# Optimization experiments

Hardware: AMD Instinct MI355X
Metric: run time of the kernel (lower is better)

Reference implementation:

```python
import jax, jax.numpy as jnp
import numpy as np

B, S, D, H = 2, 2048, 1024, 16
DK = D // H  # 64

def setup_inputs() -> dict:
    key = jax.random.key(0)
    ks = jax.random.split(key, 8)
    xavier = np.sqrt(6.0 / (D + D))  # xavier_uniform bound for square Linear
    def lin_w(k):
        return jax.random.uniform(k, (D, D), jnp.float32, -xavier, xavier)
    return {
        'Q': jax.random.normal(ks[0], (B, S, D), jnp.float32),
        'length': jax.random.randint(ks[1], (B,), 1, S + 1, jnp.int32),
        'Wq': lin_w(ks[2]), 'bq': jnp.zeros((D,), jnp.float32),
        'Wk': lin_w(ks[3]), 'bk': jnp.zeros((D,), jnp.float32),
        'Wv': lin_w(ks[4]), 'bv': jnp.zeros((D,), jnp.float32),
    }

def reference(Q, length, Wq, bq, Wk, bk, Wv, bv):
    # project and split heads: [B,S,D] -> [B,H,S,DK]
    def heads(x, W, b):
        y = jnp.einsum('bsd,de->bse', x, W) + b
        return y.reshape(B, S, H, DK).transpose(0, 2, 1, 3)
    q = heads(Q, Wq, bq)
    k = heads(Q, Wk, bk)
    v = heads(Q, Wv, bv)
    scores = jnp.einsum('bhqd,bhkd->bhqk', q, k) / np.sqrt(DK)
    scores = jnp.exp(scores)  # NOTE: raw exp, no max-subtraction (faithful)
    # multiplicative key mask: mask[b,k] = k < length[b], broadcast over q,h
    mask = (jnp.arange(S)[None, :] < length[:, None]).astype(scores.dtype)
    scores = scores * mask[:, None, None, :]
    attn = scores / (jnp.sum(scores, axis=-1, keepdims=True) + 1e-8)
    ctx = jnp.einsum('bhqk,bhkd->bhqd', attn, v)
    return ctx.transpose(0, 2, 1, 3).reshape(B, S, D)
```

## Files before the change

kernel.cpp:

```cpp
#include <hip/hip_runtime.h>
#include <hip/hip_bf16.h>

#define B_  2
#define S_  2048
#define D_  1024
#define H_  16
#define DK_ 64
#define M_  (B_ * S_)

typedef short short8 __attribute__((ext_vector_type(8)));
typedef float float4v __attribute__((ext_vector_type(4)));

static __device__ __forceinline__ ushort f32_to_bf16bits(float f) {
    union { __hip_bfloat16 h; ushort u; } cv;
    cv.h = __float2bfloat16(f);
    return cv.u;
}

static __device__ __forceinline__ void glds16(const ushort* g, ushort* l) {
    __builtin_amdgcn_global_load_lds(
        (const __attribute__((address_space(1))) unsigned int*)g,
        (__attribute__((address_space(3))) unsigned int*)l, 16, 0, 0);
}

__global__ __launch_bounds__(256) void prep(
    const float* __restrict__ X, const float* __restrict__ W0,
    const float* __restrict__ W1, const float* __restrict__ W2,
    ushort* __restrict__ Xb, ushort* __restrict__ Wt)
{
    const int z = blockIdx.z;
    const int t = threadIdx.x;

    if (z >= 3) {
        const int blk = (z - 3) * 256 + blockIdx.y * 16 + blockIdx.x;
        const int i = blk * 2048 + t * 8;
        float4v a = *(const float4v*)(X + i);
        float4v b = *(const float4v*)(X + i + 4);
        short8 o;
        o[0] = (short)f32_to_bf16bits(a[0]); o[1] = (short)f32_to_bf16bits(a[1]);
        o[2] = (short)f32_to_bf16bits(a[2]); o[3] = (short)f32_to_bf16bits(a[3]);
        o[4] = (short)f32_to_bf16bits(b[0]); o[5] = (short)f32_to_bf16bits(b[1]);
        o[6] = (short)f32_to_bf16bits(b[2]); o[7] = (short)f32_to_bf16bits(b[3]);
        *(short8*)(Xb + i) = o;
        return;
    }

    const float* W = (z == 0) ? W0 : ((z == 1) ? W1 : W2);
    ushort* out = Wt + (size_t)z * D_ * D_;

    __shared__ ushort tile[64 * 72];
    int n0 = blockIdx.x * 64, k0 = blockIdx.y * 64;
    int r = t >> 3, g = t & 7;

    #pragma unroll
    for (int p = 0; p < 2; ++p) {
        int rr = r + p * 32;
        const float* src = W + (size_t)(k0 + rr) * D_ + n0 + g * 8;
        float4v a = *(const float4v*)src;
        float4v b = *(const float4v*)(src + 4);
        short8 o;
        o[0] = (short)f32_to_bf16bits(a[0]); o[1] = (short)f32_to_bf16bits(a[1]);
        o[2] = (short)f32_to_bf16bits(a[2]); o[3] = (short)f32_to_bf16bits(a[3]);
        o[4] = (short)f32_to_bf16bits(b[0]); o[5] = (short)f32_to_bf16bits(b[1]);
        o[6] = (short)f32_to_bf16bits(b[2]); o[7] = (short)f32_to_bf16bits(b[3]);
        *(short8*)&tile[rr * 72 + g * 8] = o;
    }
    __syncthreads();
    #pragma unroll
    for (int p = 0; p < 2; ++p) {
        int rr = r + p * 32;
        short8 v;
        #pragma unroll
        for (int i = 0; i < 8; ++i)
            v[i] = (short)tile[(g * 8 + i) * 72 + rr];
        *(short8*)(out + (size_t)(n0 + rr) * D_ + k0 + g * 8) = v;
    }
}

__global__ __launch_bounds__(256) void proj_gemm(
    const ushort* __restrict__ X,
    const ushort* __restrict__ Wt,
    const float* __restrict__ b0, const float* __restrict__ b1,
    const float* __restrict__ b2,
    const int* __restrict__ length,
    ushort* __restrict__ qkv)
{
    const int z = blockIdx.z;
    const int m0 = blockIdx.x * 64, n0 = blockIdx.y * 128;

    if (z >= 1) {
        const int bidx = m0 >> 11;
        const int s0 = m0 & (S_ - 1);
        if (s0 >= length[bidx]) return;
    }

    const ushort* Wtz  = Wt + (size_t)z * D_ * D_;
    const float* bias = (z == 0) ? b0 : ((z == 1) ? b1 : b2);
    ushort* out = qkv + (size_t)z * M_ * D_;

    __shared__ ushort As[64 * 64];
    __shared__ ushort Bs[128 * 64];

    const int t = threadIdx.x;
    const int lane = t & 63, wid = t >> 6;
    const int quad = lane >> 4, l16 = lane & 15;
    const int wr = wid >> 1, wc = wid & 1;

    float4v acc[2][4] = {};

    for (int k0 = 0; k0 < D_; k0 += 64) {
        __syncthreads();
        #pragma unroll
        for (int j = 0; j < 2; ++j) {
            const int cid = wid * 128 + j * 64 + lane;
            const int row = cid >> 3;
            const int cl  = (cid & 7) ^ (row & 7);
            glds16(X + (size_t)(m0 + row) * D_ + k0 + cl * 8, &As[cid * 8]);
        }
        #pragma unroll
        for (int j = 0; j < 4; ++j) {
            const int cid = wid * 256 + j * 64 + lane;
            const int row = cid >> 3;
            const int cl  = (cid & 7) ^ (row & 7);
            glds16(Wtz + (size_t)(n0 + row) * D_ + k0 + cl * 8, &Bs[cid * 8]);
        }
        __syncthreads();

        #pragma unroll
        for (int ks = 0; ks < 2; ++ks) {
            short8 a[2], bb[4];
            #pragma unroll
            for (int i = 0; i < 2; ++i) {
                const int r = wr * 32 + i * 16 + l16;
                const int ph = (ks * 4 + quad) ^ (r & 7);
                a[i] = *(short8*)&As[r * 64 + ph * 8];
            }
            #pragma unroll
            for (int j = 0; j < 4; ++j) {
                const int r = wc * 64 + j * 16 + l16;
                const int ph = (ks * 4 + quad) ^ (r & 7);
                bb[j] = *(short8*)&Bs[r * 64 + ph * 8];
            }
            #pragma unroll
            for (int i = 0; i < 2; ++i)
                #pragma unroll
                for (int j = 0; j < 4; ++j)
                    acc[i][j] = __builtin_amdgcn_mfma_f32_16x16x32_bf16(
                        a[i], bb[j], acc[i][j], 0, 0, 0);
        }
    }

    #pragma unroll
    for (int j = 0; j < 4; ++j) {
        const int col = n0 + wc * 64 + j * 16 + l16;
        const float bv = bias[col];
        const int h = col >> 6, dk = col & (DK_ - 1);
        #pragma unroll
        for (int i = 0; i < 2; ++i) {
            #pragma unroll
            for (int rr = 0; rr < 4; ++rr) {
                const int row = m0 + wr * 32 + i * 16 + quad * 4 + rr;
                const int bidx = row >> 11;
                const int s = row & (S_ - 1);
                const float v = acc[i][j][rr] + bv;
                size_t addr;
                if (z == 2)
                    addr = ((size_t)(bidx * H_ + h) * DK_ + dk) * S_ + s;
                else
                    addr = ((size_t)(bidx * H_ + h) * S_ + s) * DK_ + dk;
                out[addr] = f32_to_bf16bits(v);
            }
        }
    }
}

__global__ __launch_bounds__(256) void attention(
    const ushort* __restrict__ qkv, const int* __restrict__ length,
    float* __restrict__ out)
{
    const int b = blockIdx.z, h = blockIdx.y, q0 = blockIdx.x * 64;
    int len = length[b];
    if (len > S_) len = S_;
    if (len < 1) len = 1;
    const int nkt = (len + 63) >> 6;

    const ushort* qb = qkv + ((size_t)(b * H_ + h) * S_ + q0) * DK_;
    const ushort* kb = qkv + (size_t)M_ * D_ + (size_t)(b * H_ + h) * S_ * DK_;
    const ushort* vb = qkv + (size_t)2 * M_ * D_ + (size_t)(b * H_ + h) * DK_ * S_;

    __shared__ ushort Qs[64 * 64];
    __shared__ ushort Ks[64 * 64];
    __shared__ ushort Vs[64 * 64];
    __shared__ ushort Ps[64 * 64];

    const int t = threadIdx.x, lane = t & 63, wid = t >> 6;
    const int quad = lane >> 4, l16 = lane & 15;
    const int qr = wid * 16 + l16;

    #pragma unroll
    for (int j = 0; j < 2; ++j) {
        const int cid = wid * 128 + j * 64 + lane;
        const int row = cid >> 3;
        const int cl  = (cid & 7) ^ (row & 7);
        glds16(qb + (size_t)row * DK_ + cl * 8, &Qs[cid * 8]);
    }

    float4v cacc[4] = {};
    float rs[4] = {};

    for (int kt = 0; kt < nkt; ++kt) {
        __syncthreads();
        #pragma unroll
        for (int j = 0; j < 2; ++j) {
            const int cid = wid * 128 + j * 64 + lane;
            const int row = cid >> 3;
            const int cl  = (cid & 7) ^ (row & 7);
            glds16(kb + (size_t)(kt * 64 + row) * DK_ + cl * 8, &Ks[cid * 8]);
            glds16(vb + (size_t)row * S_ + kt * 64 + cl * 8,    &Vs[cid * 8]);
        }
        __syncthreads();

        float4v sacc[4] = {};
        #pragma unroll
        for (int ks = 0; ks < 2; ++ks) {
            const int pha = (ks * 4 + quad) ^ (qr & 7);
            short8 a = *(short8*)&Qs[qr * 64 + pha * 8];
            #pragma unroll
            for (int ct = 0; ct < 4; ++ct) {
                const int kr = ct * 16 + l16;
                const int phb = (ks * 4 + quad) ^ (kr & 7);
                short8 bb = *(short8*)&Ks[kr * 64 + phb * 8];
                sacc[ct] = __builtin_amdgcn_mfma_f32_16x16x32_bf16(
                    a, bb, sacc[ct], 0, 0, 0);
            }
        }

        #pragma unroll
        for (int ct = 0; ct < 4; ++ct) {
            const int key = kt * 64 + ct * 16 + l16;
            const int c   = ct * 2 + (l16 >> 3);
            #pragma unroll
            for (int rr = 0; rr < 4; ++rr) {
                const int prow = wid * 16 + quad * 4 + rr;
                float val = 0.f;
                if (key < len) val = __expf(sacc[ct][rr] * 0.125f);
                rs[rr] += val;
                const int ph = c ^ (prow & 7);
                Ps[prow * 64 + ph * 8 + (l16 & 7)] = f32_to_bf16bits(val);
            }
        }

        #pragma unroll
        for (int ks = 0; ks < 2; ++ks) {
            const int pha = (ks * 4 + quad) ^ (qr & 7);
            short8 ap = *(short8*)&Ps[qr * 64 + pha * 8];
            #pragma unroll
            for (int ct = 0; ct < 4; ++ct) {
                const int vr = ct * 16 + l16;
                const int phb = (ks * 4 + quad) ^ (vr & 7);
                short8 vv = *(short8*)&Vs[vr * 64 + phb * 8];
                cacc[ct] = __builtin_amdgcn_mfma_f32_16x16x32_bf16(
                    ap, vv, cacc[ct], 0, 0, 0);
            }
        }
    }

    #pragma unroll
    for (int rr = 0; rr < 4; ++rr) {
        float v = rs[rr];
        #pragma unroll
        for (int off = 1; off < 16; off <<= 1)
            v += __shfl_xor(v, off, 16);
        rs[rr] = v;
    }

    #pragma unroll
    for (int ct = 0; ct < 4; ++ct)
        #pragma unroll
        for (int rr = 0; rr < 4; ++rr) {
            const int q = q0 + wid * 16 + quad * 4 + rr;
            const int d = h * 64 + ct * 16 + l16;
            out[((size_t)b * S_ + q) * D_ + d] = cacc[ct][rr] / (rs[rr] + 1e-8f);
        }
}

extern "C" void kernel_launch(void* const* d_in, const int* in_sizes, int n_in,
                              void* d_out, int out_size, void* d_ws, size_t ws_size,
                              hipStream_t stream)
{
    const float* Q   = (const float*)d_in[0];
    const int*   len = (const int*)d_in[1];
    const float* Wq  = (const float*)d_in[2];
    const float* bq  = (const float*)d_in[3];
    const float* Wk  = (const float*)d_in[4];
    const float* bk  = (const float*)d_in[5];
    const float* Wv  = (const float*)d_in[6];
    const float* bv  = (const float*)d_in[7];
    float* out = (float*)d_out;

    ushort* ws  = (ushort*)d_ws;
    ushort* Xb  = ws;
    ushort* Wt  = ws + (size_t)M_ * D_;
    ushort* qkv = Wt + (size_t)3 * D_ * D_;

    dim3 gPr(16, 16, 11);
    prep<<<gPr, 256, 0, stream>>>(Q, Wq, Wk, Wv, Xb, Wt);

    dim3 gP(M_ / 64, D_ / 128, 3);
    proj_gemm<<<gP, 256, 0, stream>>>(Xb, Wt, bq, bk, bv, len, qkv);

    dim3 gA(S_ / 64, H_, B_);
    attention<<<gA, 256, 0, stream>>>(qkv, len, out);
}
```

Baseline: 177.0 us.

## Double-buffer GEMM and attention tiles, fold softmax scale into Q, use exp2

Double-buffers the LDS tiles in both the projection GEMM and the attention kernel, so the next K/V or A/B tile is fetched while the current one is computed, with one barrier per iteration. Q is pre-scaled by log2(e)/sqrt(dk) in the projection epilogue so attention can call the hardware exp2 directly. The score MFMA operands are swapped so each lane holds four consecutive keys for one query row; P is written as packed bf16 pairs and the row sum becomes a short cross-lane reduction. Masking is skipped for full tiles, launch bounds gain an occupancy hint, and the doubled LDS use may reduce occupancy.

```diff
diff --git a/kernel.cpp b/kernel.cpp
--- a/kernel.cpp
+++ b/kernel.cpp
@@ -11,10 +11,15 @@
 typedef short short8 __attribute__((ext_vector_type(8)));
 typedef float float4v __attribute__((ext_vector_type(4)));
 
+#define QSCALE 0.18033688011112042f
+
 static __device__ __forceinline__ ushort f32_to_bf16bits(float f) {
     union { __hip_bfloat16 h; ushort u; } cv;
     cv.h = __float2bfloat16(f);
     return cv.u;
+}
+static __device__ __forceinline__ unsigned pk2(float a, float b) {
+    return (unsigned)f32_to_bf16bits(a) | ((unsigned)f32_to_bf16bits(b) << 16);
 }
 
 static __device__ __forceinline__ void glds16(const ushort* g, ushort* l) {
@@ -77,7 +82,7 @@
     }
 }
 
-__global__ __launch_bounds__(256) void proj_gemm(
+__global__ __launch_bounds__(256, 3) void proj_gemm(
     const ushort* __restrict__ X,
     const ushort* __restrict__ Wt,
     const float* __restrict__ b0, const float* __restrict__ b1,
@@ -98,8 +103,8 @@
     const float* bias = (z == 0) ? b0 : ((z == 1) ? b1 : b2);
     ushort* out = qkv + (size_t)z * M_ * D_;
 
-    __shared__ ushort As[64 * 64];
-    __shared__ ushort Bs[128 * 64];
+    __shared__ __align__(16) ushort As[2][64 * 64];
+    __shared__ __align__(16) ushort Bs[2][128 * 64];
 
     const int t = threadIdx.x;
     const int lane = t & 63, wid = t >> 6;
@@ -108,23 +113,41 @@
 
     float4v acc[2][4] = {};
 
-    for (int k0 = 0; k0 < D_; k0 += 64) {
-        __syncthreads();
-        #pragma unroll
-        for (int j = 0; j < 2; ++j) {
-            const int cid = wid * 128 + j * 64 + lane;
-            const int row = cid >> 3;
-            const int cl  = (cid & 7) ^ (row & 7);
-            glds16(X + (size_t)(m0 + row) * D_ + k0 + cl * 8, &As[cid * 8]);
-        }
-        #pragma unroll
-        for (int j = 0; j < 4; ++j) {
-            const int cid = wid * 256 + j * 64 + lane;
-            const int row = cid >> 3;
-            const int cl  = (cid & 7) ^ (row & 7);
-            glds16(Wtz + (size_t)(n0 + row) * D_ + k0 + cl * 8, &Bs[cid * 8]);
-        }
-        __syncthreads();
+    #pragma unroll
+    for (int j = 0; j < 2; ++j) {
+        const int cid = wid * 128 + j * 64 + lane;
+        const int row = cid >> 3;
+        const int cl  = (cid & 7) ^ (row & 7);
+        glds16(X + (size_t)(m0 + row) * D_ + cl * 8, &As[0][cid * 8]);
+    }
+    #pragma unroll
+    for (int j = 0; j < 4; ++j) {
+        const int cid = wid * 256 + j * 64 + lane;
+        const int row = cid >> 3;
+        const int cl  = (cid & 7) ^ (row & 7);
+        glds16(Wtz + (size_t)(n0 + row) * D_ + cl * 8, &Bs[0][cid * 8]);
+    }
+    __syncthreads();
+
+    for (int kt = 0; kt < 16; ++kt) {
+        const int cur = kt & 1, nxt = cur ^ 1;
+        if (kt + 1 < 16) {
+            const int k0 = (kt + 1) * 64;
+            #pragma unroll
+            for (int j = 0; j < 2; ++j) {
+                const int cid = wid * 128 + j * 64 + lane;
+                const int row = cid >> 3;
+                const int cl  = (cid & 7) ^ (row & 7);
+                glds16(X + (size_t)(m0 + row) * D_ + k0 + cl * 8, &As[nxt][cid * 8]);
+            }
+            #pragma unroll
+            for (int j = 0; j < 4; ++j) {
+                const int cid = wid * 256 + j * 64 + lane;
+                const int row = cid >> 3;
+                const int cl  = (cid & 7) ^ (row & 7);
+                glds16(Wtz + (size_t)(n0 + row) * D_ + k0 + cl * 8, &Bs[nxt][cid * 8]);
+            }
+        }
 
         #pragma unroll
         for (int ks = 0; ks < 2; ++ks) {
@@ -133,13 +156,13 @@
             for (int i = 0; i < 2; ++i) {
                 const int r = wr * 32 + i * 16 + l16;
                 const int ph = (ks * 4 + quad) ^ (r & 7);
-                a[i] = *(short8*)&As[r * 64 + ph * 8];
+                a[i] = *(short8*)&As[cur][r * 64 + ph * 8];
             }
             #pragma unroll
             for (int j = 0; j < 4; ++j) {
                 const int r = wc * 64 + j * 16 + l16;
                 const int ph = (ks * 4 + quad) ^ (r & 7);
-                bb[j] = *(short8*)&Bs[r * 64 + ph * 8];
+                bb[j] = *(short8*)&Bs[cur][r * 64 + ph * 8];
             }
             #pragma unroll
             for (int i = 0; i < 2; ++i)
@@ -148,8 +171,10 @@
                     acc[i][j] = __builtin_amdgcn_mfma_f32_16x16x32_bf16(
                         a[i], bb[j], acc[i][j], 0, 0, 0);
         }
-    }
-
+        __syncthreads();
+    }
+
+    const float sc = (z == 0) ? QSCALE : 1.0f;
     #pragma unroll
     for (int j = 0; j < 4; ++j) {
         const int col = n0 + wc * 64 + j * 16 + l16;
@@ -162,7 +187,7 @@
                 const int row = m0 + wr * 32 + i * 16 + quad * 4 + rr;
                 const int bidx = row >> 11;
                 const int s = row & (S_ - 1);
-                const float v = acc[i][j][rr] + bv;
+                const float v = (acc[i][j][rr] + bv) * sc;
                 size_t addr;
                 if (z == 2)
                     addr = ((size_t)(bidx * H_ + h) * DK_ + dk) * S_ + s;
@@ -174,7 +199,7 @@
     }
 }
 
-__global__ __launch_bounds__(256) void attention(
+__global__ __launch_bounds__(256, 3) void attention(
     const ushort* __restrict__ qkv, const int* __restrict__ length,
     float* __restrict__ out)
 {
@@ -188,14 +213,15 @@
     const ushort* kb = qkv + (size_t)M_ * D_ + (size_t)(b * H_ + h) * S_ * DK_;
     const ushort* vb = qkv + (size_t)2 * M_ * D_ + (size_t)(b * H_ + h) * DK_ * S_;
 
-    __shared__ ushort Qs[64 * 64];
-    __shared__ ushort Ks[64 * 64];
-    __shared__ ushort Vs[64 * 64];
-    __shared__ ushort Ps[64 * 64];
+    __shared__ __align__(16) ushort Qs[64 * 64];
+    __shared__ __align__(16) ushort Ks[2][64 * 64];
+    __shared__ __align__(16) ushort Vs[2][64 * 64];
+    __shared__ __align__(16) ushort Ps[64 * 64];
 
     const int t = threadIdx.x, lane = t & 63, wid = t >> 6;
     const int quad = lane >> 4, l16 = lane & 15;
-    const int qr = wid * 16 + l16;
+    const int qrow = wid * 16 + l16;
+    const int e8 = (l16 & 7) << 1;
 
     #pragma unroll
     for (int j = 0; j < 2; ++j) {
@@ -203,85 +229,96 @@
         const int row = cid >> 3;
         const int cl  = (cid & 7) ^ (row & 7);
         glds16(qb + (size_t)row * DK_ + cl * 8, &Qs[cid * 8]);
-    }
+        glds16(kb + (size_t)row * DK_ + cl * 8, &Ks[0][cid * 8]);
+        glds16(vb + (size_t)row * S_ + cl * 8,  &Vs[0][cid * 8]);
+    }
+    __syncthreads();
 
     float4v cacc[4] = {};
-    float rs[4] = {};
+    float rs = 0.f;
 
     for (int kt = 0; kt < nkt; ++kt) {
-        __syncthreads();
-        #pragma unroll
-        for (int j = 0; j < 2; ++j) {
-            const int cid = wid * 128 + j * 64 + lane;
-            const int row = cid >> 3;
-            const int cl  = (cid & 7) ^ (row & 7);
-            glds16(kb + (size_t)(kt * 64 + row) * DK_ + cl * 8, &Ks[cid * 8]);
-            glds16(vb + (size_t)row * S_ + kt * 64 + cl * 8,    &Vs[cid * 8]);
-        }
-        __syncthreads();
+        const int cur = kt & 1, nxt = cur ^ 1;
+        if (kt + 1 < nkt) {
+            #pragma unroll
+            for (int j = 0; j < 2; ++j) {
+                const int cid = wid * 128 + j * 64 + lane;
+                const int row = cid >> 3;
+                const int cl  = (cid & 7) ^ (row & 7);
+                glds16(kb + (size_t)((kt + 1) * 64 + row) * DK_ + cl * 8,
+                       &Ks[nxt][cid * 8]);
+                glds16(vb + (size_t)row * S_ + (kt + 1) * 64 + cl * 8,
+                       &Vs[nxt][cid * 8]);
+            }
+        }
 
         float4v sacc[4] = {};
         #pragma unroll
         for (int ks = 0; ks < 2; ++ks) {
-            const int pha = (ks * 4 + quad) ^ (qr & 7);
-            short8 a = *(short8*)&Qs[qr * 64 + pha * 8];
+            const int phb = (ks * 4 + quad) ^ (l16 & 7);
+            short8 bq8 = *(short8*)&Qs[qrow * 64 + phb * 8];
             #pragma unroll
             for (int ct = 0; ct < 4; ++ct) {
-                const int kr = ct * 16 + l16;
-                const int phb = (ks * 4 + quad) ^ (kr & 7);
-                short8 bb = *(short8*)&Ks[kr * 64 + phb * 8];
+                const int krow = ct * 16 + l16;
+                const int pha = (ks * 4 + quad) ^ (krow & 7);
+                short8 ak = *(short8*)&Ks[cur][krow * 64 + pha * 8];
                 sacc[ct] = __builtin_amdgcn_mfma_f32_16x16x32_bf16(
-                    a, bb, sacc[ct], 0, 0, 0);
-            }
-        }
-
+                    ak, bq8, sacc[ct], 0, 0, 0);
+            }
+        }
+
+        const bool full = ((kt + 1) * 64 <= len);
         #pragma unroll
         for (int ct = 0; ct < 4; ++ct) {
-            const int key = kt * 64 + ct * 16 + l16;
-            const int c   = ct * 2 + (l16 >> 3);
-            #pragma unroll
-            for (int rr = 0; rr < 4; ++rr) {
-                const int prow = wid * 16 + quad * 4 + rr;
-                float val = 0.f;
-                if (key < len) val = __expf(sacc[ct][rr] * 0.125f);
-                rs[rr] += val;
-                const int ph = c ^ (prow & 7);
-                Ps[prow * 64 + ph * 8 + (l16 & 7)] = f32_to_bf16bits(val);
-            }
+            float v0 = __builtin_amdgcn_exp2f(sacc[ct][0]);
+            float v1 = __builtin_amdgcn_exp2f(sacc[ct][1]);
+            float v2 = __builtin_amdgcn_exp2f(sacc[ct][2]);
+            float v3 = __builtin_amdgcn_exp2f(sacc[ct][3]);
+            if (!full) {
+                const int kb0 = kt * 64 + ct * 16 + quad * 4;
+                v0 = (kb0 + 0 < len) ? v0 : 0.f;
+                v1 = (kb0 + 1 < len) ? v1 : 0.f;
+                v2 = (kb0 + 2 < len) ? v2 : 0.f;
+                v3 = (kb0 + 3 < len) ? v3 : 0.f;
+            }
+            rs += (v0 + v1) + (v2 + v3);
+            uint2 w;
+            w.x = pk2(v0, v1);
+            w.y = pk2(v2, v3);
+            const int c8 = (ct * 4 + quad) ^ e8;
+            *(uint2*)&Ps[qrow * 64 + c8 * 4] = w;
         }
 
         #pragma unroll
         for (int ks = 0; ks < 2; ++ks) {
-            const int pha = (ks * 4 + quad) ^ (qr & 7);
-            short8 ap = *(short8*)&Ps[qr * 64 + pha * 8];
+            const int pp = ((ks * 4 + quad) * 2) ^ e8;
+            short8 ap = *(short8*)&Ps[qrow * 64 + pp * 4];
             #pragma unroll
             for (int ct = 0; ct < 4; ++ct) {
-                const int vr = ct * 16 + l16;
-                const int phb = (ks * 4 + quad) ^ (vr & 7);
-                short8 vv = *(short8*)&Vs[vr * 64 + phb * 8];
+                const int vrow = ct * 16 + l16;
+                const int phv = (ks * 4 + quad) ^ (vrow & 7);
+                short8 vv = *(short8*)&Vs[cur][vrow * 64 + phv * 8];
                 cacc[ct] = __builtin_amdgcn_mfma_f32_16x16x32_bf16(
                     ap, vv, cacc[ct], 0, 0, 0);
             }
         }
-    }
+        __syncthreads();
+    }
+
+    rs += __shfl_xor(rs, 16);
+    rs += __shfl_xor(rs, 32);
 
     #pragma unroll
     for (int rr = 0; rr < 4; ++rr) {
-        float v = rs[rr];
-        #pragma unroll
-        for (int off = 1; off < 16; off <<= 1)
-            v += __shfl_xor(v, off, 16);
-        rs[rr] = v;
-    }
-
-    #pragma unroll
-    for (int ct = 0; ct < 4; ++ct)
-        #pragma unroll
-        for (int rr = 0; rr < 4; ++rr) {
-            const int q = q0 + wid * 16 + quad * 4 + rr;
+        const float rsq = __shfl(rs, quad * 4 + rr, 16);
+        const float inv = 1.0f / (rsq + 1e-8f);
+        const int q = q0 + wid * 16 + quad * 4 + rr;
+        #pragma unroll
+        for (int ct = 0; ct < 4; ++ct) {
             const int d = h * 64 + ct * 16 + l16;
-            out[((size_t)b * S_ + q) * D_ + d] = cacc[ct][rr] / (rs[rr] + 1e-8f);
-        }
+            out[((size_t)b * S_ + q) * D_ + d] = cacc[ct][rr] * inv;
+        }
+    }
 }
 
 extern "C" void kernel_launch(void* const* d_in, const int* in_sizes, int n_in,
```

Measured after the change: 167.8 us. 5.2% less time.
